# Performance work log

Measured on AMD Instinct MI355X. Metric: run time of the kernel, lower is better.

## Reference

```python
import jax, jax.numpy as jnp
import numpy as np
from jax import lax

BLANK = 0
B, T, U, V = 8, 256, 64, 512  # U1 = U + 1


def setup_inputs() -> dict:
    key = jax.random.key(0)
    k1, k2, k3 = jax.random.split(key, 3)
    enc_state = jax.random.normal(k1, (B, T, V), dtype=jnp.float32)
    dec_state = jax.random.normal(k2, (B, U + 1, V), dtype=jnp.float32)
    # targets are non-blank labels in [1, V)
    targets = jax.random.randint(k3, (B, U), 1, V, dtype=jnp.int32)
    input_lengths = jnp.full((B,), T, dtype=jnp.int32)
    target_lengths = jnp.full((B,), U, dtype=jnp.int32)
    return {"enc_state": enc_state, "dec_state": dec_state, "targets": targets,
            "input_lengths": input_lengths, "target_lengths": target_lengths}


def rnnt_loss(logits, targets, input_lengths, target_lengths, blank=BLANK):
    # logits: [B, T, U1, V]; targets: [B, U]
    b, t_len, u1, v = logits.shape
    u_len = u1 - 1
    lp = jax.nn.log_softmax(logits, axis=-1)
    blank_lp = lp[..., blank]                                   # [B, T, U1]
    idx = jnp.broadcast_to(targets[:, None, :, None], (b, t_len, u_len, 1))
    emit_lp = jnp.take_along_axis(lp[:, :, :u_len, :], idx, axis=3)[..., 0]  # [B, T, U]

    # alpha[0, u] = sum_{k<u} emit_lp[0, k]
    alpha0 = jnp.concatenate(
        [jnp.zeros((b, 1), lp.dtype), jnp.cumsum(emit_lp[:, 0, :], axis=1)], axis=1)  # [B, U1]

    def t_step(alpha_prev, xs):
        blank_prev, emit_t = xs  # [B, U1], [B, U]
        init = alpha_prev + blank_prev  # contribution from (t-1, u) blank transition

        def u_step(carry, x):
            init_u, emit_u = x  # each [B]
            a = jnp.logaddexp(init_u, carry + emit_u)  # a[u] = lse(init[u], a[u-1]+emit[u-1])
            return a, a

        _, rest = lax.scan(u_step, init[:, 0], (init[:, 1:].T, emit_t.T))  # rest: [U, B]
        alpha_t = jnp.concatenate([init[:, :1], rest.T], axis=1)  # [B, U1]
        return alpha_t, alpha_t

    xs = (blank_lp[:, :t_len - 1].transpose(1, 0, 2), emit_lp[:, 1:].transpose(1, 0, 2))
    _, alphas_rest = lax.scan(t_step, alpha0, xs)
    alphas = jnp.concatenate([alpha0[None], alphas_rest], axis=0)  # [T, B, U1]

    bi = jnp.arange(b)
    tl = target_lengths.astype(jnp.int32)
    il = input_lengths.astype(jnp.int32)
    a_final = alphas[il - 1, bi, tl]
    final_blank = blank_lp[bi, il - 1, tl]
    nll = -(a_final + final_blank)
    return jnp.mean(nll)  # reduction='mean'


def reference(enc_state, dec_state, targets, input_lengths, target_lengths):
    # JointNet: broadcast-add enc [B,T,1,V] + dec [B,1,U1,V] -> logits [B,T,U1,V]
    logits = enc_state[:, :, None, :] + dec_state[:, None, :, :]
    return rnnt_loss(logits, targets, input_lengths, target_lengths, blank=BLANK)
```

## Files before the change

### kernel.cpp

```cpp
#include <hip/hip_runtime.h>

#define B_ 8
#define T_ 256
#define U_ 64
#define U1_ 65
#define V_ 512
#define NDIAGP_ 336
#define NT_ 2
#define CH_ 64

#define LOG2E_ 1.4426950408889634f
#define LN2_   0.6931471805599453f

#if __has_builtin(__builtin_amdgcn_exp2f)
#define EXP2(x) __builtin_amdgcn_exp2f(x)
#else
#define EXP2(x) exp2f(x)
#endif

template <int CTRL, int RM>
__device__ __forceinline__ float dppadd(float x) {
    return x + __int_as_float(__builtin_amdgcn_update_dpp(
        0, __float_as_int(x), CTRL, RM, 0xf, true));
}
__device__ __forceinline__ float wave_sum64(float x) {
    x = dppadd<0x111, 0xf>(x);
    x = dppadd<0x112, 0xf>(x);
    x = dppadd<0x114, 0xf>(x);
    x = dppadd<0x118, 0xf>(x);
    x = dppadd<0x142, 0xa>(x);
    x = dppadd<0x143, 0xc>(x);
    return x;
}

__global__ __launch_bounds__(256) void k_logprobs(
    const float* __restrict__ enc, const float* __restrict__ dec,
    const int* __restrict__ targets,
    float* __restrict__ BLD, float* __restrict__ EMD,
    float* __restrict__ out)
{
    const int blk  = blockIdx.x;
    const int b    = blk % B_;
    const int tg   = blk / B_;
    const int t0   = tg * NT_;
    const int wave = threadIdx.x >> 6;
    const int lane = threadIdx.x & 63;

    if (blk == 0 && threadIdx.x == 0) out[0] = 0.0f;

    float4 xe0[NT_], xe1[NT_];
    float  er0[NT_];
    #pragma unroll
    for (int j = 0; j < NT_; ++j) {
        const float* erow = enc + (size_t)(b * T_ + t0 + j) * V_;
        float4 e0 = *(const float4*)(erow + lane * 4);
        float4 e1 = *(const float4*)(erow + 256 + lane * 4);
        xe0[j].x = __expf(e0.x); xe0[j].y = __expf(e0.y);
        xe0[j].z = __expf(e0.z); xe0[j].w = __expf(e0.w);
        xe1[j].x = __expf(e1.x); xe1[j].y = __expf(e1.y);
        xe1[j].z = __expf(e1.z); xe1[j].w = __expf(e1.w);
        er0[j] = erow[0];
    }

    for (int u = wave; u <= U_; u += 4) {
        const float* drow = dec + (size_t)(b * U1_ + u) * V_;
        float4 d0 = *(const float4*)(drow + lane * 4);
        float4 d1 = *(const float4*)(drow + 256 + lane * 4);
        d0.x = __expf(d0.x); d0.y = __expf(d0.y);
        d0.z = __expf(d0.z); d0.w = __expf(d0.w);
        d1.x = __expf(d1.x); d1.y = __expf(d1.y);
        d1.z = __expf(d1.z); d1.w = __expf(d1.w);

        float s[NT_];
        #pragma unroll
        for (int j = 0; j < NT_; ++j) {
            float sA = xe0[j].x * d0.x;
            float sB = xe1[j].x * d1.x;
            sA = fmaf(xe0[j].y, d0.y, sA);  sB = fmaf(xe1[j].y, d1.y, sB);
            sA = fmaf(xe0[j].z, d0.z, sA);  sB = fmaf(xe1[j].z, d1.z, sB);
            sA = fmaf(xe0[j].w, d0.w, sA);  sB = fmaf(xe1[j].w, d1.w, sB);
            s[j] = sA + sB;
        }

        #pragma unroll
        for (int j = 0; j < NT_; ++j)
            s[j] = wave_sum64(s[j]);

        if (lane == 63) {
            const float d_blank = drow[0];
            int   tgt = 0;
            float d_tgt = 0.0f;
            if (u < U_) { tgt = targets[b * U_ + u]; d_tgt = drow[tgt]; }
            #pragma unroll
            for (int j = 0; j < NT_; ++j) {
                const int t  = t0 + j;
                const int dg = t + u;
                const float lse2 = log2f(s[j]);
                BLD[((size_t)b * NDIAGP_ + dg) * U1_ + u] =
                    (er0[j] + d_blank) * LOG2E_ - lse2;
                if (u < U_) {
                    const float* er = enc + (size_t)(b * T_ + t) * V_;
                    EMD[((size_t)b * NDIAGP_ + dg) * U_ + u] =
                        (er[tgt] + d_tgt) * LOG2E_ - lse2;
                }
            }
        }
    }
}

__device__ __forceinline__ float wshr1(float x) {
    return __int_as_float(__builtin_amdgcn_update_dpp(
        0, __float_as_int(x), 0x138, 0xf, 0xf, true));
}
template <int CTRL>
__device__ __forceinline__ float dppmax(float x) {
    return fmaxf(x, __int_as_float(__builtin_amdgcn_update_dpp(
        0, __float_as_int(x), CTRL, 0xf, 0xf, false)));
}
__device__ __forceinline__ float wave_max64(float x) {
    x = dppmax<0x111>(x);
    x = dppmax<0x112>(x);
    x = dppmax<0x114>(x);
    x = dppmax<0x118>(x);
    x = dppmax<0x142>(x);
    x = dppmax<0x143>(x);
    return __int_as_float(__builtin_amdgcn_readlane(__float_as_int(x), 63));
}

#define GLDS(c_) do {                                                           \
    if (wave > 0) {                                                             \
        const float* gbl = BLb + (size_t)(c_) * CH_ * U1_;                      \
        const float* gem = EMb + (size_t)(c_) * CH_ * U_;                       \
        float* lbl_ = sRBL[(c_) & 1];                                           \
        float* lem_ = sREM[(c_) & 1];                                           \
        for (int i = wave - 1; i < 17; i += 7)                                  \
            __builtin_amdgcn_global_load_lds(                                   \
                (const __attribute__((address_space(1))) void*)(gbl + i * 256 + lane * 4), \
                (__attribute__((address_space(3))) void*)(lbl_ + i * 256), 16, 0, 0);      \
        for (int i = wave - 1; i < 16; i += 7)                                  \
            __builtin_amdgcn_global_load_lds(                                   \
                (const __attribute__((address_space(1))) void*)(gem + i * 256 + lane * 4), \
                (__attribute__((address_space(3))) void*)(lem_ + i * 256), 16, 0, 0);      \
    }                                                                           \
} while (0)

#define CONV(c_) do {                                                           \
    if (wave > 0) {                                                             \
        const float* rbl = sRBL[(c_) & 1];                                      \
        const float* rem = sREM[(c_) & 1];                                      \
        float4* pv_ = sPV[(c_) & 1];                                            \
        float*  pc_ = sPC[(c_) & 1];                                            \
        _Pragma("unroll 3")                                                     \
        for (int i = wave - 1; i < CH_; i += 7) {                               \
            const float bl = rbl[i * U1_ + lane + 1];                           \
            const float em = rem[i * U_ + lane];                                \
            const float pc = ((c_) == 4) ? rbl[i * U1_ + i + 1]                 \
                                         : rbl[i * U1_];                        \
            float vb = fminf(bl - pc, 126.0f);                                  \
            float ve = fminf(em - pc, 126.0f);                                  \
            if ((c_) == 0 && lane == i) vb = -200.0f;                           \
            if ((c_) == 4 && lane <= i) { vb = -200.0f; ve = -200.0f; }         \
            ((float2*)&pv_[(i >> 1) * 64 + lane])[i & 1] =                      \
                make_float2(EXP2(vb), EXP2(ve));                                \
            if (lane == 0) pc_[i] = pc;                                         \
        }                                                                       \
    }                                                                           \
} while (0)

#define LOADG(PV, PCQ, g_) do {                                                 \
    _Pragma("unroll")                                                           \
    for (int k = 0; k < 4; ++k)                                                 \
        PV[k] = pvb[(4 * (g_) + k) * 64 + lane];                                \
    PCQ[0] = pcb4[2 * (g_)];                                                    \
    PCQ[1] = pcb4[2 * (g_) + 1];                                                \
} while (0)

#define PCSEL(PCQ, j_) ((j_) < 4 ? ((j_) == 0 ? PCQ[0].x : (j_) == 1 ? PCQ[0].y \
                                  : (j_) == 2 ? PCQ[0].z : PCQ[0].w)            \
                                 : ((j_) == 4 ? PCQ[1].x : (j_) == 5 ? PCQ[1].y \
                                  : (j_) == 6 ? PCQ[1].z : PCQ[1].w))

#define COMPG(PV, PCQ, g_) do {                                                 \
    _Pragma("unroll")                                                           \
    for (int j = 0; j < 8; ++j) {                                               \
        const int d = d0 + 8 * (g_) + j + 1;                                    \
        const float pbv = (j & 1) ? PV[j >> 1].z : PV[j >> 1].x;                \
        const float pev = (j & 1) ? PV[j >> 1].w : PV[j >> 1].y;                \
        const float pcj = PCSEL(PCQ, j);                                        \
        float sr = wshr1(r);                                                    \
        sr = lane0 ? r0 : sr;                                                   \
        r = fmaf(sr, pev, r * pbv);                                             \
        const bool cap = (d == cap_d);                                          \
        savedV = cap ? (tlpos ? r : r0) : savedV;                               \
        savedC = cap ? (tlpos ? Rc + pcj : Rc) : savedC;                        \
        Rc += pcj;                                                              \
    }                                                                           \
    {                                                                           \
        float m = wave_max64(r);                                                \
        int mb = __float_as_int(m);                                             \
        int e = (mb >> 23) - 127;                                               \
        e = (mb >= 0x00800000) ? e : 0;                                         \
        float sc = __int_as_float((127 - e) << 23);                             \
        r *= sc;  r0 *= sc;  Rc += (float)e;                                    \
    }                                                                           \
} while (0)

#define CHUNK_BODY(c_) do {                                                     \
    const float4* pvb  = sPV[(c_) & 1];                                         \
    const float4* pcb4 = (const float4*)sPC[(c_) & 1];                          \
    const int d0 = CH_ * (c_);                                                  \
    float4 pvA[4], pvB[4];                                                      \
    float4 pcA[2], pcB[2];                                                      \
    LOADG(pvA, pcA, 0);                                                         \
    for (int g = 0; g < 8; g += 2) {                                            \
        LOADG(pvB, pcB, g + 1);                                                 \
        COMPG(pvA, pcA, g);                                                     \
        if (g + 2 < 8) LOADG(pvA, pcA, g + 2);                                  \
        COMPG(pvB, pcB, g + 1);                                                 \
    }                                                                           \
} while (0)

__global__ __launch_bounds__(512) void k_alpha(
    const float* __restrict__ BLD, const float* __restrict__ EMD,
    const int* __restrict__ il_, const int* __restrict__ tl_,
    float* __restrict__ sink)
{
    __shared__ __align__(16) float  sRBL[2][17 * 256];
    __shared__ __align__(16) float  sREM[2][16 * 256];
    __shared__ __align__(16) float4 sPV[2][32 * 64];
    __shared__ __align__(16) float  sPC[2][CH_];

    const int b    = blockIdx.x;
    const int wave = threadIdx.x >> 6;
    const int lane = threadIdx.x & 63;
    const int il   = il_[b];
    const int tl   = tl_[b];
    const int dstar = il - 1 + tl;
    const float* BLb = BLD + (size_t)b * NDIAGP_ * U1_;
    const float* EMb = EMD + (size_t)b * NDIAGP_ * U_;
    const float fblank = BLb[(size_t)dstar * U1_ + tl];

    const bool lane0 = (lane == 0);
    const bool tlpos = (tl > 0);
    const int  cap_d = tlpos ? dstar : il;

    float r  = 0.0f;
    float r0 = 1.0f;
    float Rc = 0.0f;
    float savedV = 1.0f, savedC = 0.0f;

    GLDS(0);
    __syncthreads();
    GLDS(1);
    CONV(0);
    __syncthreads();

    for (int c = 0; c < 5; ++c) {
        if (c + 2 <= 4) GLDS(c + 2);
        if (c + 1 <= 4) CONV(c + 1);
        if (wave == 0) { CHUNK_BODY(c); }
        __syncthreads();
    }

    if (wave == 0) {
        const int sl = tlpos ? (tl - 1) : 0;
        float sv = __int_as_float(
            __builtin_amdgcn_readlane(__float_as_int(savedV), sl));
        float sc = __int_as_float(
            __builtin_amdgcn_readlane(__float_as_int(savedC), 0));
        if (lane == 0)
            atomicAdd(sink, -(sc + log2f(sv) + fblank) * (LN2_ / B_));
    }
}

extern "C" void kernel_launch(void* const* d_in, const int* in_sizes, int n_in,
                              void* d_out, int out_size, void* d_ws, size_t ws_size,
                              hipStream_t stream)
{
    const float* enc     = (const float*)d_in[0];
    const float* dec     = (const float*)d_in[1];
    const int*   targets = (const int*)d_in[2];
    const int*   il      = (const int*)d_in[3];
    const int*   tl      = (const int*)d_in[4];
    float*       out     = (float*)d_out;

    float* BLD = (float*)d_ws;
    float* EMD = BLD + (size_t)B_ * NDIAGP_ * U1_;

    k_logprobs<<<B_ * T_ / NT_, 256, 0, stream>>>(enc, dec, targets, BLD, EMD, out);
    k_alpha<<<B_, 512, 0, stream>>>(BLD, EMD, il, tl, out);
}
```

Measured before the change: 37.94 us.

## Precompute all diagonal transition weights as packed bf16 in LDS upfront

```diff
diff --git a/kernel.cpp b/kernel.cpp
--- a/kernel.cpp
+++ b/kernel.cpp
@@ -7,7 +7,7 @@
 #define V_ 512
 #define NDIAGP_ 336
 #define NT_ 2
-#define CH_ 64
+#define ND_ 320
 
 #define LOG2E_ 1.4426950408889634f
 #define LN2_   0.6931471805599453f
@@ -31,6 +31,24 @@
     x = dppadd<0x142, 0xa>(x);
     x = dppadd<0x143, 0xc>(x);
     return x;
+}
+__device__ __forceinline__ float wshr1(float x) {
+    return __int_as_float(__builtin_amdgcn_update_dpp(
+        0, __float_as_int(x), 0x138, 0xf, 0xf, true));
+}
+template <int CTRL>
+__device__ __forceinline__ float dppmax(float x) {
+    return fmaxf(x, __int_as_float(__builtin_amdgcn_update_dpp(
+        0, __float_as_int(x), CTRL, 0xf, 0xf, false)));
+}
+__device__ __forceinline__ float wave_max64(float x) {
+    x = dppmax<0x111>(x);
+    x = dppmax<0x112>(x);
+    x = dppmax<0x114>(x);
+    x = dppmax<0x118>(x);
+    x = dppmax<0x142>(x);
+    x = dppmax<0x143>(x);
+    return __int_as_float(__builtin_amdgcn_readlane(__float_as_int(x), 63));
 }
 
 __global__ __launch_bounds__(256) void k_logprobs(
@@ -108,71 +126,12 @@
     }
 }
 
-__device__ __forceinline__ float wshr1(float x) {
-    return __int_as_float(__builtin_amdgcn_update_dpp(
-        0, __float_as_int(x), 0x138, 0xf, 0xf, true));
-}
-template <int CTRL>
-__device__ __forceinline__ float dppmax(float x) {
-    return fmaxf(x, __int_as_float(__builtin_amdgcn_update_dpp(
-        0, __float_as_int(x), CTRL, 0xf, 0xf, false)));
-}
-__device__ __forceinline__ float wave_max64(float x) {
-    x = dppmax<0x111>(x);
-    x = dppmax<0x112>(x);
-    x = dppmax<0x114>(x);
-    x = dppmax<0x118>(x);
-    x = dppmax<0x142>(x);
-    x = dppmax<0x143>(x);
-    return __int_as_float(__builtin_amdgcn_readlane(__float_as_int(x), 63));
-}
-
-#define GLDS(c_) do {                                                           \
-    if (wave > 0) {                                                             \
-        const float* gbl = BLb + (size_t)(c_) * CH_ * U1_;                      \
-        const float* gem = EMb + (size_t)(c_) * CH_ * U_;                       \
-        float* lbl_ = sRBL[(c_) & 1];                                           \
-        float* lem_ = sREM[(c_) & 1];                                           \
-        for (int i = wave - 1; i < 17; i += 7)                                  \
-            __builtin_amdgcn_global_load_lds(                                   \
-                (const __attribute__((address_space(1))) void*)(gbl + i * 256 + lane * 4), \
-                (__attribute__((address_space(3))) void*)(lbl_ + i * 256), 16, 0, 0);      \
-        for (int i = wave - 1; i < 16; i += 7)                                  \
-            __builtin_amdgcn_global_load_lds(                                   \
-                (const __attribute__((address_space(1))) void*)(gem + i * 256 + lane * 4), \
-                (__attribute__((address_space(3))) void*)(lem_ + i * 256), 16, 0, 0);      \
-    }                                                                           \
-} while (0)
-
-#define CONV(c_) do {                                                           \
-    if (wave > 0) {                                                             \
-        const float* rbl = sRBL[(c_) & 1];                                      \
-        const float* rem = sREM[(c_) & 1];                                      \
-        float4* pv_ = sPV[(c_) & 1];                                            \
-        float*  pc_ = sPC[(c_) & 1];                                            \
-        _Pragma("unroll 3")                                                     \
-        for (int i = wave - 1; i < CH_; i += 7) {                               \
-            const float bl = rbl[i * U1_ + lane + 1];                           \
-            const float em = rem[i * U_ + lane];                                \
-            const float pc = ((c_) == 4) ? rbl[i * U1_ + i + 1]                 \
-                                         : rbl[i * U1_];                        \
-            float vb = fminf(bl - pc, 126.0f);                                  \
-            float ve = fminf(em - pc, 126.0f);                                  \
-            if ((c_) == 0 && lane == i) vb = -200.0f;                           \
-            if ((c_) == 4 && lane <= i) { vb = -200.0f; ve = -200.0f; }         \
-            ((float2*)&pv_[(i >> 1) * 64 + lane])[i & 1] =                      \
-                make_float2(EXP2(vb), EXP2(ve));                                \
-            if (lane == 0) pc_[i] = pc;                                         \
-        }                                                                       \
-    }                                                                           \
-} while (0)
-
-#define LOADG(PV, PCQ, g_) do {                                                 \
+#define LOADG(PW, PCQ, g_) do {                                                 \
     _Pragma("unroll")                                                           \
-    for (int k = 0; k < 4; ++k)                                                 \
-        PV[k] = pvb[(4 * (g_) + k) * 64 + lane];                                \
-    PCQ[0] = pcb4[2 * (g_)];                                                    \
-    PCQ[1] = pcb4[2 * (g_) + 1];                                                \
+    for (int j = 0; j < 8; ++j)                                                 \
+        PW[j] = sPV[(8 * (g_) + j) * 64 + lane];                                \
+    PCQ[0] = pc4[2 * (g_)];                                                     \
+    PCQ[1] = pc4[2 * (g_) + 1];                                                 \
 } while (0)
 
 #define PCSEL(PCQ, j_) ((j_) < 4 ? ((j_) == 0 ? PCQ[0].x : (j_) == 1 ? PCQ[0].y \
@@ -180,12 +139,13 @@
                                  : ((j_) == 4 ? PCQ[1].x : (j_) == 5 ? PCQ[1].y \
                                   : (j_) == 6 ? PCQ[1].z : PCQ[1].w))
 
-#define COMPG(PV, PCQ, g_) do {                                                 \
+#define COMPG(PW, PCQ, g_) do {                                                 \
     _Pragma("unroll")                                                           \
     for (int j = 0; j < 8; ++j) {                                               \
-        const int d = d0 + 8 * (g_) + j + 1;                                    \
-        const float pbv = (j & 1) ? PV[j >> 1].z : PV[j >> 1].x;                \
-        const float pev = (j & 1) ? PV[j >> 1].w : PV[j >> 1].y;                \
+        const int d = 8 * (g_) + j + 1;                                         \
+        const unsigned int w = PW[j];                                           \
+        const float pbv = __uint_as_float(w & 0xffff0000u);                     \
+        const float pev = __uint_as_float(w << 16);                             \
         const float pcj = PCSEL(PCQ, j);                                        \
         float sr = wshr1(r);                                                    \
         sr = lane0 ? r0 : sr;                                                   \
@@ -195,7 +155,7 @@
         savedC = cap ? (tlpos ? Rc + pcj : Rc) : savedC;                        \
         Rc += pcj;                                                              \
     }                                                                           \
-    {                                                                           \
+    {                               \
         float m = wave_max64(r);                                                \
         int mb = __float_as_int(m);                                             \
         int e = (mb >> 23) - 127;                                               \
@@ -205,30 +165,13 @@
     }                                                                           \
 } while (0)
 
-#define CHUNK_BODY(c_) do {                                                     \
-    const float4* pvb  = sPV[(c_) & 1];                                         \
-    const float4* pcb4 = (const float4*)sPC[(c_) & 1];                          \
-    const int d0 = CH_ * (c_);                                                  \
-    float4 pvA[4], pvB[4];                                                      \
-    float4 pcA[2], pcB[2];                                                      \
-    LOADG(pvA, pcA, 0);                                                         \
-    for (int g = 0; g < 8; g += 2) {                                            \
-        LOADG(pvB, pcB, g + 1);                                                 \
-        COMPG(pvA, pcA, g);                                                     \
-        if (g + 2 < 8) LOADG(pvA, pcA, g + 2);                                  \
-        COMPG(pvB, pcB, g + 1);                                                 \
-    }                                                                           \
-} while (0)
-
 __global__ __launch_bounds__(512) void k_alpha(
     const float* __restrict__ BLD, const float* __restrict__ EMD,
     const int* __restrict__ il_, const int* __restrict__ tl_,
-    float* __restrict__ sink)
+    float* __restrict__ out)
 {
-    __shared__ __align__(16) float  sRBL[2][17 * 256];
-    __shared__ __align__(16) float  sREM[2][16 * 256];
-    __shared__ __align__(16) float4 sPV[2][32 * 64];
-    __shared__ __align__(16) float  sPC[2][CH_];
+    __shared__ __align__(16) unsigned int sPV[ND_ * 64];
+    __shared__ __align__(16) float sPC[ND_];
 
     const int b    = blockIdx.x;
     const int wave = threadIdx.x >> 6;
@@ -238,7 +181,32 @@
     const int dstar = il - 1 + tl;
     const float* BLb = BLD + (size_t)b * NDIAGP_ * U1_;
     const float* EMb = EMD + (size_t)b * NDIAGP_ * U_;
-    const float fblank = BLb[(size_t)dstar * U1_ + tl];
+
+    for (int kb = 0; kb < 40; kb += 8) {
+        float bl[8], em[8], pcv[8];
+        #pragma unroll
+        for (int j = 0; j < 8; ++j) {
+            const int row = wave + 8 * (kb + j);
+            const int rc  = row < 256 ? 0 : row - 255;
+            bl[j]  = BLb[(size_t)row * U1_ + lane + 1];
+            em[j]  = EMb[(size_t)row * U_ + lane];
+            pcv[j] = BLb[(size_t)row * U1_ + rc];
+        }
+        #pragma unroll
+        for (int j = 0; j < 8; ++j) {
+            const int row = wave + 8 * (kb + j);
+            float vb = fminf(bl[j] - pcv[j], 126.0f);
+            float ve = fminf(em[j] - pcv[j], 126.0f);
+            if (row < 64 && lane == row) vb = -200.0f;
+            if (row >= 256 && lane <= row - 256) { vb = -200.0f; ve = -200.0f; }
+            const unsigned int ub = __float_as_uint(EXP2(vb)) + 0x8000u;
+            const unsigned int ue = __float_as_uint(EXP2(ve)) + 0x8000u;
+            sPV[row * 64 + lane] = (ub & 0xffff0000u) | (ue >> 16);
+            if (lane == 0) sPC[row] = pcv[j];
+        }
+    }
+    __syncthreads();
+    if (wave != 0) return;
 
     const bool lane0 = (lane == 0);
     const bool tlpos = (tl > 0);
@@ -249,27 +217,28 @@
     float Rc = 0.0f;
     float savedV = 1.0f, savedC = 0.0f;
 
-    GLDS(0);
-    __syncthreads();
-    GLDS(1);
-    CONV(0);
-    __syncthreads();
-
-    for (int c = 0; c < 5; ++c) {
-        if (c + 2 <= 4) GLDS(c + 2);
-        if (c + 1 <= 4) CONV(c + 1);
-        if (wave == 0) { CHUNK_BODY(c); }
-        __syncthreads();
-    }
-
-    if (wave == 0) {
+    const float4* pc4 = (const float4*)sPC;
+    unsigned int pwA[8], pwB[8];
+    float4 pcA[2], pcB[2];
+
+    LOADG(pwA, pcA, 0);
+    for (int g = 0; g < 40; g += 2) {
+        LOADG(pwB, pcB, g + 1);
+        COMPG(pwA, pcA, g);
+        if (g + 2 < 40) LOADG(pwA, pcA, g + 2);
+        COMPG(pwB, pcB, g + 1);
+    }
+
+    {
         const int sl = tlpos ? (tl - 1) : 0;
         float sv = __int_as_float(
             __builtin_amdgcn_readlane(__float_as_int(savedV), sl));
         float sc = __int_as_float(
             __builtin_amdgcn_readlane(__float_as_int(savedC), 0));
-        if (lane == 0)
-            atomicAdd(sink, -(sc + log2f(sv) + fblank) * (LN2_ / B_));
+        if (lane == 0) {
+            const float fblank = BLb[(size_t)dstar * U1_ + tl];
+            atomicAdd(out, -(sc + log2f(sv) + fblank) * (LN2_ / B_));
+        }
     }
 }
 
```

Measured after the change: 39.62 us. +4.4%, slower.
